# Kernel tuning notes

Measured on AMD Instinct MI355X. Metric: run time of the kernel, lower is better.

Reference implementation:

```python
import jax, jax.numpy as jnp
import numpy as np

B, S, D, H = 4, 2048, 1024, 16
DH = D // H


def setup_inputs() -> dict:
    key = jax.random.key(0)
    ks = jax.random.split(key, 11)
    s = 1.0 / np.sqrt(D)
    return {
        "q": jax.random.normal(ks[0], (B, S, D), jnp.float32),
        "k": jax.random.normal(ks[1], (B, S, D), jnp.float32),
        "v": jax.random.normal(ks[2], (B, S, D), jnp.float32),
        "Wq": jax.random.normal(ks[3], (D, D), jnp.float32) * s,
        "bq": jnp.zeros((D,), jnp.float32),
        "Wk": jax.random.normal(ks[4], (D, D), jnp.float32) * s,
        "bk": jnp.zeros((D,), jnp.float32),
        "Wv": jax.random.normal(ks[5], (D, D), jnp.float32) * s,
        "bv": jnp.zeros((D,), jnp.float32),
        "Wo": jax.random.normal(ks[6], (D, D), jnp.float32) * s,
        "bo": jnp.zeros((D,), jnp.float32),
    }


def _split_heads(x):
    # (B, S, D) -> (B, H, S, DH)
    b, s, _ = x.shape
    return x.reshape(b, s, H, DH).transpose(0, 2, 1, 3)


def reference(q, k, v, Wq, bq, Wk, bk, Wv, bv, Wo, bo):
    # torch Linear: x @ W.T + b
    qh = _split_heads(q @ Wq.T + bq)
    kh = _split_heads(k @ Wk.T + bk)
    vh = _split_heads(v @ Wv.T + bv)
    scale = 1.0 / jnp.sqrt(jnp.asarray(DH, qh.dtype))
    scores = jnp.einsum("bhqd,bhkd->bhqk", qh, kh) * scale  # (B,H,S,S)
    probs = jax.nn.softmax(scores, axis=-1)
    ctx = jnp.einsum("bhqk,bhkd->bhqd", probs, vh)  # (B,H,S,DH)
    x = ctx.transpose(0, 2, 1, 3).reshape(q.shape[0], -1, D)
    return x @ Wo.T + bo
```

## Files before the change

### kernel.cpp

```cpp
#include <hip/hip_runtime.h>

typedef __bf16 bf16x8 __attribute__((ext_vector_type(8)));
typedef __bf16 bf16x4 __attribute__((ext_vector_type(4)));
typedef _Float16 f16x8 __attribute__((ext_vector_type(8)));
typedef _Float16 f16x4v __attribute__((ext_vector_type(4)));
typedef float f32x4 __attribute__((ext_vector_type(4)));
typedef float f32x16 __attribute__((ext_vector_type(16)));
typedef unsigned short u16;
typedef unsigned int u32;
typedef unsigned int u32x4 __attribute__((ext_vector_type(4)));

constexpr int Bc = 4, Sc = 2048, Dc = 1024, Hc = 16, DHc = 64;
constexpr int Mrows = Bc * Sc;
constexpr size_t MK = (size_t)Mrows * Dc;
constexpr size_t WK = (size_t)Dc * Dc;

__device__ __forceinline__ u16 f2bf(float f) {
  u32 u = __float_as_uint(f);
  u = (u + 0x7fffu + ((u >> 16) & 1u)) >> 16;
  return (u16)u;
}

#define LDSP(p) ((__attribute__((address_space(3))) void*)(p))
#define GLBP(p) ((const __attribute__((address_space(1))) void*)(p))

__global__ __launch_bounds__(256) void cvt3_kernel(const float* __restrict__ a,
                                                   const float* __restrict__ b,
                                                   const float* __restrict__ c,
                                                   ushort4* __restrict__ out, int n4) {
  const float4* in = (const float4*)(blockIdx.y == 0 ? a : blockIdx.y == 1 ? b : c);
  ushort4* o = out + (size_t)blockIdx.y * n4;
  int stride = gridDim.x * blockDim.x;
  for (int i = blockIdx.x * blockDim.x + threadIdx.x; i < n4; i += stride) {
    float4 v = in[i];
    ushort4 r;
    r.x = f2bf(v.x); r.y = f2bf(v.y); r.z = f2bf(v.z); r.w = f2bf(v.w);
    o[i] = r;
  }
}

__global__ __launch_bounds__(256) void cvt4_kernel(const float* __restrict__ a,
                                                   const float* __restrict__ b,
                                                   const float* __restrict__ c,
                                                   const float* __restrict__ d,
                                                   ushort4* __restrict__ out, int n4) {
  const float4* in = (const float4*)(blockIdx.y == 0 ? a : blockIdx.y == 1 ? b
                                     : blockIdx.y == 2 ? c : d);
  ushort4* o = out + (size_t)blockIdx.y * n4;
  int stride = gridDim.x * blockDim.x;
  for (int i = blockIdx.x * blockDim.x + threadIdx.x; i < n4; i += stride) {
    float4 v = in[i];
    ushort4 r;
    r.x = f2bf(v.x); r.y = f2bf(v.y); r.z = f2bf(v.z); r.w = f2bf(v.w);
    o[i] = r;
  }
}

template <int FUSED3>
__global__ __launch_bounds__(512, 2) void gemm8(const u16* __restrict__ A0,
                                                const u16* __restrict__ Bt0,
                                                const float* __restrict__ b0,
                                                const float* __restrict__ b1,
                                                const float* __restrict__ b2,
                                                void* __restrict__ out0) {
  constexpr int K = 1024, NT = 16;
  __shared__ u16 lds[3 * 24576];

  const int y = FUSED3 ? (int)blockIdx.y : 3;
  const u16* A = A0 + (FUSED3 ? (size_t)blockIdx.y * MK : 0);
  const u16* Bt = Bt0 + (FUSED3 ? (size_t)blockIdx.y * WK : 0);
  const float* bias = FUSED3 ? (y == 0 ? b0 : y == 1 ? b1 : b2) : b0;

  const int wg = (blockIdx.x & 7) * 32 + (blockIdx.x >> 3);
  const int tm = wg >> 3, tn = wg & 7;
  const int row0 = tm << 8, col0 = tn << 7;

  const int t_ = threadIdx.x, w = t_ >> 6, l = t_ & 63;
  const int wm = w >> 1, wn = w & 1;
  const int col = l & 31, hh = l >> 5;

  f32x16 acc[2][2] = {};

  auto stA = [&](int tile, int i) {
    u16* buf = &lds[(tile % 3) * 24576];
    const int c = (w * 4 + i) * 64 + l;
    const int r = c >> 3, gl = c & 7;
    __builtin_amdgcn_global_load_lds(
        GLBP(A + (size_t)(row0 + r) * K + (tile << 6) + ((gl ^ (r & 7)) << 3)),
        LDSP(buf + (w * 4 + i) * 512), 16, 0, 0);
  };
  auto stB = [&](int tile, int i) {
    u16* buf = &lds[(tile % 3) * 24576] + 16384;
    const int c = (w * 2 + i) * 64 + l;
    const int r = c >> 3, gl = c & 7;
    __builtin_amdgcn_global_load_lds(
        GLBP(Bt + (size_t)(col0 + r) * K + (tile << 6) + ((gl ^ (r & 7)) << 3)),
        LDSP(buf + (w * 2 + i) * 512), 16, 0, 0);
  };

#pragma unroll
  for (int i = 0; i < 4; ++i) stA(0, i);
#pragma unroll
  for (int i = 0; i < 2; ++i) stB(0, i);
#pragma unroll
  for (int i = 0; i < 4; ++i) stA(1, i);
#pragma unroll
  for (int i = 0; i < 2; ++i) stB(1, i);
  asm volatile("s_waitcnt vmcnt(6)" ::: "memory");
  __builtin_amdgcn_s_barrier();

  const int ar0 = wm * 64 + col, ar1 = ar0 + 32;
  const int br0 = wn * 64 + col, br1 = br0 + 32;

#pragma unroll 1
  for (int t = 0; t < NT; ++t) {
    const u16* abuf = &lds[(t % 3) * 24576];
    const u16* bbuf = abuf + 16384;
#pragma unroll
    for (int ph = 0; ph < 2; ++ph) {
      bf16x8 a0[2], a1[2], q0[2], q1[2];
#pragma unroll
      for (int k2 = 0; k2 < 2; ++k2) {
        const int ks = ph * 2 + k2;
        a0[k2] = *(const bf16x8*)&abuf[ar0 * 64 + ((((ks << 1) + hh) ^ (ar0 & 7)) << 3)];
        a1[k2] = *(const bf16x8*)&abuf[ar1 * 64 + ((((ks << 1) + hh) ^ (ar1 & 7)) << 3)];
        q0[k2] = *(const bf16x8*)&bbuf[br0 * 64 + ((((ks << 1) + hh) ^ (br0 & 7)) << 3)];
        q1[k2] = *(const bf16x8*)&bbuf[br1 * 64 + ((((ks << 1) + hh) ^ (br1 & 7)) << 3)];
      }
      if (t + 2 < NT) {
        if (ph == 0) { stA(t + 2, 0); stA(t + 2, 1); stA(t + 2, 2); }
        else         { stA(t + 2, 3); stB(t + 2, 0); stB(t + 2, 1); }
      }
      __builtin_amdgcn_sched_barrier(0);
      __builtin_amdgcn_s_barrier();
      __builtin_amdgcn_sched_barrier(0);
      __builtin_amdgcn_s_setprio(1);
#pragma unroll
      for (int k2 = 0; k2 < 2; ++k2) {
        acc[0][0] = __builtin_amdgcn_mfma_f32_32x32x16_bf16(a0[k2], q0[k2], acc[0][0], 0, 0, 0);
        acc[0][1] = __builtin_amdgcn_mfma_f32_32x32x16_bf16(a0[k2], q1[k2], acc[0][1], 0, 0, 0);
        acc[1][0] = __builtin_amdgcn_mfma_f32_32x32x16_bf16(a1[k2], q0[k2], acc[1][0], 0, 0, 0);
        acc[1][1] = __builtin_amdgcn_mfma_f32_32x32x16_bf16(a1[k2], q1[k2], acc[1][1], 0, 0, 0);
      }
      __builtin_amdgcn_s_setprio(0);
      __builtin_amdgcn_sched_barrier(0);
    }
    if (t + 2 < NT)      asm volatile("s_waitcnt vmcnt(6)" ::: "memory");
    else if (t + 1 < NT) asm volatile("s_waitcnt vmcnt(0)" ::: "memory");
    __builtin_amdgcn_s_barrier();
  }

#pragma unroll
  for (int mi = 0; mi < 2; ++mi)
#pragma unroll
    for (int ni = 0; ni < 2; ++ni) {
      const int n = col0 + wn * 64 + ni * 32 + col;
      const float bv = bias[n];
      const int mbase = row0 + wm * 64 + mi * 32 + 4 * hh;
      if (y == 3) {
        float* O = (float*)out0;
#pragma unroll
        for (int r = 0; r < 16; ++r) {
          const int m = mbase + (r & 3) + 8 * (r >> 2);
          O[(size_t)m * Dc + n] = acc[mi][ni][r] + bv;
        }
      } else if (y == 2) {
        u16* Vt = (u16*)out0 + 2 * MK;
        const int h = n >> 6, dh = n & 63;
#pragma unroll
        for (int qg = 0; qg < 4; ++qg) {
          const int s0 = mbase + 8 * qg;
          const int b = s0 >> 11, s = s0 & (Sc - 1);
          f16x4v pk;
#pragma unroll
          for (int r4 = 0; r4 < 4; ++r4) pk[r4] = (_Float16)(acc[mi][ni][qg * 4 + r4] + bv);
          *(f16x4v*)&Vt[((size_t)((b * Hc + h) * DHc + dh)) * Sc + s] = pk;
        }
      } else {
        u16* Oh = (u16*)out0 + (size_t)y * MK;
        const float scl = (y == 0) ? 0.125f * 1.44269504089f : 1.f;
        const int h = n >> 6, dh = n & 63;
#pragma unroll
        for (int r = 0; r < 16; ++r) {
          const int m = mbase + (r & 3) + 8 * (r >> 2);
          const int b = m >> 11, s = m & (Sc - 1);
          Oh[((size_t)((b * Hc + h) * Sc + s)) * DHc + dh] = f2bf((acc[mi][ni][r] + bv) * scl);
        }
      }
    }
}

__global__ __launch_bounds__(256, 4) void attn4_kernel(const u16* __restrict__ Qh,
                                                       const u16* __restrict__ Kh,
                                                       const u16* __restrict__ Vt,
                                                       u16* __restrict__ ctx) {
  __shared__ u16 smem[16384];
  u16* K_lds = smem;
  u16* V_lds = smem + 8192;

  const int wid = (blockIdx.x & 7) * 128 + (blockIdx.x >> 3);
  const int qt = wid & 15, bh = wid >> 4;
  const int t = threadIdx.x, w = t >> 6, l = t & 63;
  const int q = l & 31, h = l >> 5;
  const int q0 = qt * 128 + w * 32;

  bf16x8 qf[4];
  {
    const u16* qp = Qh + ((size_t)bh * Sc + q0 + q) * DHc + h * 8;
#pragma unroll
    for (int kk = 0; kk < 4; ++kk) qf[kk] = *(const bf16x8*)(qp + kk * 16);
  }

  f32x16 oacc[2] = {};
  float m_run = -3.0e38f, l_run = 0.f;

  const int lrow = l >> 3, lg = l & 7;

  auto stage = [&](int tile, int buf) {
    const int kt = tile << 6;
    u16* Kb = K_lds + buf * 4096;
    u16* Vb = V_lds + buf * 4096;
#pragma unroll
    for (int c = 0; c < 2; ++c) {
      const int rb = w * 16 + c * 8;
      const int row = rb + lrow;
      const int sg = lg ^ (row & 7);
      __builtin_amdgcn_global_load_lds(GLBP(Kh + ((size_t)bh * Sc + kt + row) * DHc + sg * 8),
                                       LDSP(&Kb[rb * 64]), 16, 0, 0);
      __builtin_amdgcn_global_load_lds(GLBP(Vt + ((size_t)bh * DHc + row) * Sc + kt + sg * 8),
                                       LDSP(&Vb[rb * 64]), 16, 0, 0);
    }
  };

  stage(0, 0);
  __syncthreads();

#pragma unroll 1
  for (int tile = 0; tile < 32; ++tile) {
    const int cur = tile & 1;
    if (tile + 1 < 32) stage(tile + 1, cur ^ 1);
    const u16* Kb = K_lds + cur * 4096;
    const u16* Vb = V_lds + cur * 4096;

    f32x16 sacc[2] = {};
    __builtin_amdgcn_s_setprio(1);
#pragma unroll
    for (int kk = 0; kk < 4; ++kk) {
      const int kr0 = q, kr1 = 32 + q;
      bf16x8 kf0 = *(const bf16x8*)&Kb[kr0 * 64 + ((2 * kk + h) ^ (kr0 & 7)) * 8];
      bf16x8 kf1 = *(const bf16x8*)&Kb[kr1 * 64 + ((2 * kk + h) ^ (kr1 & 7)) * 8];
      sacc[0] = __builtin_amdgcn_mfma_f32_32x32x16_bf16(kf0, qf[kk], sacc[0], 0, 0, 0);
      sacc[1] = __builtin_amdgcn_mfma_f32_32x32x16_bf16(kf1, qf[kk], sacc[1], 0, 0, 0);
    }
    __builtin_amdgcn_s_setprio(0);

    float mx = sacc[0][0];
#pragma unroll
    for (int r = 1; r < 16; ++r) mx = fmaxf(mx, sacc[0][r]);
#pragma unroll
    for (int r = 0; r < 16; ++r) mx = fmaxf(mx, sacc[1][r]);
    mx = fmaxf(mx, __shfl_xor(mx, 32));
    if (__any(mx - m_run > 8.f)) {
      const float mnew = fmaxf(m_run, mx);
      const float corr = __builtin_amdgcn_exp2f(m_run - mnew);
      m_run = mnew;
      l_run *= corr;
#pragma unroll
      for (int dt = 0; dt < 2; ++dt)
#pragma unroll
        for (int r = 0; r < 16; ++r) oacc[dt][r] *= corr;
    }

    float sum = 0.f;
#pragma unroll
    for (int kt32 = 0; kt32 < 2; ++kt32)
#pragma unroll
      for (int c = 0; c < 2; ++c) {
        float p0 = __builtin_amdgcn_exp2f(sacc[kt32][c * 8 + 0] - m_run);
        float p1 = __builtin_amdgcn_exp2f(sacc[kt32][c * 8 + 1] - m_run);
        float p2 = __builtin_amdgcn_exp2f(sacc[kt32][c * 8 + 2] - m_run);
        float p3 = __builtin_amdgcn_exp2f(sacc[kt32][c * 8 + 3] - m_run);
        float p4 = __builtin_amdgcn_exp2f(sacc[kt32][c * 8 + 4] - m_run);
        float p5 = __builtin_amdgcn_exp2f(sacc[kt32][c * 8 + 5] - m_run);
        float p6 = __builtin_amdgcn_exp2f(sacc[kt32][c * 8 + 6] - m_run);
        float p7 = __builtin_amdgcn_exp2f(sacc[kt32][c * 8 + 7] - m_run);
        sum += ((p0 + p1) + (p2 + p3)) + ((p4 + p5) + (p6 + p7));
        u32 X0 = __builtin_bit_cast(u32, __builtin_amdgcn_cvt_pkrtz(p0, p1));
        u32 X1 = __builtin_bit_cast(u32, __builtin_amdgcn_cvt_pkrtz(p2, p3));
        u32 Y0 = __builtin_bit_cast(u32, __builtin_amdgcn_cvt_pkrtz(p4, p5));
        u32 Y1 = __builtin_bit_cast(u32, __builtin_amdgcn_cvt_pkrtz(p6, p7));
        auto rA = __builtin_amdgcn_permlane32_swap(X0, Y0, false, false);
        auto rB = __builtin_amdgcn_permlane32_swap(X1, Y1, false, false);
        u32x4 wv;
        wv[0] = rA[0]; wv[1] = rB[0]; wv[2] = rA[1]; wv[3] = rB[1];
        f16x8 pf = __builtin_bit_cast(f16x8, wv);
        const int gb = kt32 * 4 + c * 2 + h;
        __builtin_amdgcn_s_setprio(1);
#pragma unroll
        for (int dt = 0; dt < 2; ++dt) {
          const int vrow = dt * 32 + q;
          f16x8 vf = *(const f16x8*)&Vb[vrow * 64 + ((gb ^ (vrow & 7)) * 8)];
          oacc[dt] = __builtin_amdgcn_mfma_f32_32x32x16_f16(vf, pf, oacc[dt], 0, 0, 0);
        }
        __builtin_amdgcn_s_setprio(0);
      }
    sum += __shfl_xor(sum, 32);
    l_run += sum;
    __syncthreads();
  }

  const float inv = 1.f / l_run;
  u16* E = smem + w * 2048;
#pragma unroll
  for (int dt = 0; dt < 2; ++dt)
#pragma unroll
    for (int rg = 0; rg < 4; ++rg) {
      bf16x4 pk;
#pragma unroll
      for (int j = 0; j < 4; ++j) pk[j] = (__bf16)(oacc[dt][rg * 4 + j] * inv);
      const int dh0 = dt * 32 + rg * 8 + 4 * h;
      int byte = q * 128 + dh0 * 2;
      byte ^= (q & 7) << 4;
      *(bf16x4*)((char*)E + byte) = pk;
    }
  __syncthreads();
  const int b = bh >> 4, head = bh & 15;
  const size_t crow = ((size_t)(b * Sc + q0 + q)) * Dc + head * 64 + h * 32;
#pragma unroll
  for (int i = 0; i < 4; ++i) {
    const int g = (4 * h + i) ^ (q & 7);
    uint4 tv = *(const uint4*)((char*)E + q * 128 + g * 16);
    *(uint4*)((u16*)ctx + crow + i * 8) = tv;
  }
}

extern "C" void kernel_launch(void* const* d_in, const int* in_sizes, int n_in,
                              void* d_out, int out_size, void* d_ws, size_t ws_size,
                              hipStream_t stream) {
  const float* q  = (const float*)d_in[0];
  const float* k  = (const float*)d_in[1];
  const float* v  = (const float*)d_in[2];
  const float* Wq = (const float*)d_in[3];
  const float* bq = (const float*)d_in[4];
  const float* Wk = (const float*)d_in[5];
  const float* bk = (const float*)d_in[6];
  const float* Wv = (const float*)d_in[7];
  const float* bv = (const float*)d_in[8];
  const float* Wo = (const float*)d_in[9];
  const float* bo = (const float*)d_in[10];
  float* out = (float*)d_out;

  u16* qb  = (u16*)d_ws;
  u16* Wqb = qb + 3 * MK;
  u16* Qh  = Wqb + 4 * WK;
  u16* Kh  = Qh + MK;
  u16* VtB = Kh + MK;
  u16* ctx = VtB + MK;

  cvt3_kernel<<<dim3(2048, 3), 256, 0, stream>>>(q, k, v, (ushort4*)qb, (int)(MK / 4));
  cvt4_kernel<<<dim3(512, 4), 256, 0, stream>>>(Wq, Wk, Wv, Wo, (ushort4*)Wqb, (int)(WK / 4));

  gemm8<1><<<dim3(256, 3), 512, 0, stream>>>(qb, Wqb, bq, bk, bv, (void*)Qh);

  attn4_kernel<<<1024, 256, 0, stream>>>(Qh, Kh, VtB, ctx);

  gemm8<0><<<dim3(256, 1), 512, 0, stream>>>(ctx, Wqb + 3 * WK, bo, bo, bo, (void*)out);
}
```

Before: 220.5 us.

## Simplify GEMM mainloop to one barrier per tile; sum softmax probs via fdot2

The projection GEMM main loop drops its two-phase split with a mid-tile barrier. It now issues all prefetch loads for tile t+2 up front, reads all four k-slices of LDS fragments, then runs 16 MFMAs with one barrier per tile. This cuts barrier overhead but holds more fragment registers and may lose overlap of loads and compute. In attention, the row sum of exponentials uses fdot2 on the already-packed fp16 pairs instead of separate fp32 adds, which saves VALU work but sums rounded fp16 values.

```diff
diff --git a/kernel.cpp b/kernel.cpp
--- a/kernel.cpp
+++ b/kernel.cpp
@@ -4,6 +4,7 @@
 typedef __bf16 bf16x4 __attribute__((ext_vector_type(4)));
 typedef _Float16 f16x8 __attribute__((ext_vector_type(8)));
 typedef _Float16 f16x4v __attribute__((ext_vector_type(4)));
+typedef __fp16 fp16x2 __attribute__((ext_vector_type(2)));
 typedef float f32x4 __attribute__((ext_vector_type(4)));
 typedef float f32x16 __attribute__((ext_vector_type(16)));
 typedef unsigned short u16;
@@ -116,35 +117,27 @@
   for (int t = 0; t < NT; ++t) {
     const u16* abuf = &lds[(t % 3) * 24576];
     const u16* bbuf = abuf + 16384;
-#pragma unroll
-    for (int ph = 0; ph < 2; ++ph) {
-      bf16x8 a0[2], a1[2], q0[2], q1[2];
-#pragma unroll
-      for (int k2 = 0; k2 < 2; ++k2) {
-        const int ks = ph * 2 + k2;
-        a0[k2] = *(const bf16x8*)&abuf[ar0 * 64 + ((((ks << 1) + hh) ^ (ar0 & 7)) << 3)];
-        a1[k2] = *(const bf16x8*)&abuf[ar1 * 64 + ((((ks << 1) + hh) ^ (ar1 & 7)) << 3)];
-        q0[k2] = *(const bf16x8*)&bbuf[br0 * 64 + ((((ks << 1) + hh) ^ (br0 & 7)) << 3)];
-        q1[k2] = *(const bf16x8*)&bbuf[br1 * 64 + ((((ks << 1) + hh) ^ (br1 & 7)) << 3)];
-      }
-      if (t + 2 < NT) {
-        if (ph == 0) { stA(t + 2, 0); stA(t + 2, 1); stA(t + 2, 2); }
-        else         { stA(t + 2, 3); stB(t + 2, 0); stB(t + 2, 1); }
-      }
-      __builtin_amdgcn_sched_barrier(0);
-      __builtin_amdgcn_s_barrier();
-      __builtin_amdgcn_sched_barrier(0);
-      __builtin_amdgcn_s_setprio(1);
-#pragma unroll
-      for (int k2 = 0; k2 < 2; ++k2) {
-        acc[0][0] = __builtin_amdgcn_mfma_f32_32x32x16_bf16(a0[k2], q0[k2], acc[0][0], 0, 0, 0);
-        acc[0][1] = __builtin_amdgcn_mfma_f32_32x32x16_bf16(a0[k2], q1[k2], acc[0][1], 0, 0, 0);
-        acc[1][0] = __builtin_amdgcn_mfma_f32_32x32x16_bf16(a1[k2], q0[k2], acc[1][0], 0, 0, 0);
-        acc[1][1] = __builtin_amdgcn_mfma_f32_32x32x16_bf16(a1[k2], q1[k2], acc[1][1], 0, 0, 0);
-      }
-      __builtin_amdgcn_s_setprio(0);
-      __builtin_amdgcn_sched_barrier(0);
-    }
+    if (t + 2 < NT) {
+      stA(t + 2, 0); stA(t + 2, 1); stA(t + 2, 2); stA(t + 2, 3);
+      stB(t + 2, 0); stB(t + 2, 1);
+    }
+    bf16x8 af0[4], af1[4], bf0[4], bf1[4];
+#pragma unroll
+    for (int ks = 0; ks < 4; ++ks) {
+      af0[ks] = *(const bf16x8*)&abuf[ar0 * 64 + ((((ks << 1) + hh) ^ (ar0 & 7)) << 3)];
+      af1[ks] = *(const bf16x8*)&abuf[ar1 * 64 + ((((ks << 1) + hh) ^ (ar1 & 7)) << 3)];
+      bf0[ks] = *(const bf16x8*)&bbuf[br0 * 64 + ((((ks << 1) + hh) ^ (br0 & 7)) << 3)];
+      bf1[ks] = *(const bf16x8*)&bbuf[br1 * 64 + ((((ks << 1) + hh) ^ (br1 & 7)) << 3)];
+    }
+    __builtin_amdgcn_s_setprio(1);
+#pragma unroll
+    for (int ks = 0; ks < 4; ++ks) {
+      acc[0][0] = __builtin_amdgcn_mfma_f32_32x32x16_bf16(af0[ks], bf0[ks], acc[0][0], 0, 0, 0);
+      acc[0][1] = __builtin_amdgcn_mfma_f32_32x32x16_bf16(af0[ks], bf1[ks], acc[0][1], 0, 0, 0);
+      acc[1][0] = __builtin_amdgcn_mfma_f32_32x32x16_bf16(af1[ks], bf0[ks], acc[1][0], 0, 0, 0);
+      acc[1][1] = __builtin_amdgcn_mfma_f32_32x32x16_bf16(af1[ks], bf1[ks], acc[1][1], 0, 0, 0);
+    }
+    __builtin_amdgcn_s_setprio(0);
     if (t + 2 < NT)      asm volatile("s_waitcnt vmcnt(6)" ::: "memory");
     else if (t + 1 < NT) asm volatile("s_waitcnt vmcnt(0)" ::: "memory");
     __builtin_amdgcn_s_barrier();
@@ -213,6 +206,7 @@
 
   f32x16 oacc[2] = {};
   float m_run = -3.0e38f, l_run = 0.f;
+  const fp16x2 ones2 = {(__fp16)1.f, (__fp16)1.f};
 
   const int lrow = l >> 3, lg = l & 7;
 
@@ -271,7 +265,7 @@
         for (int r = 0; r < 16; ++r) oacc[dt][r] *= corr;
     }
 
-    float sum = 0.f;
+    float sumA = 0.f, sumB = 0.f;
 #pragma unroll
     for (int kt32 = 0; kt32 < 2; ++kt32)
 #pragma unroll
@@ -284,13 +278,18 @@
         float p5 = __builtin_amdgcn_exp2f(sacc[kt32][c * 8 + 5] - m_run);
         float p6 = __builtin_amdgcn_exp2f(sacc[kt32][c * 8 + 6] - m_run);
         float p7 = __builtin_amdgcn_exp2f(sacc[kt32][c * 8 + 7] - m_run);
-        sum += ((p0 + p1) + (p2 + p3)) + ((p4 + p5) + (p6 + p7));
-        u32 X0 = __builtin_bit_cast(u32, __builtin_amdgcn_cvt_pkrtz(p0, p1));
-        u32 X1 = __builtin_bit_cast(u32, __builtin_amdgcn_cvt_pkrtz(p2, p3));
-        u32 Y0 = __builtin_bit_cast(u32, __builtin_amdgcn_cvt_pkrtz(p4, p5));
-        u32 Y1 = __builtin_bit_cast(u32, __builtin_amdgcn_cvt_pkrtz(p6, p7));
-        auto rA = __builtin_amdgcn_permlane32_swap(X0, Y0, false, false);
-        auto rB = __builtin_amdgcn_permlane32_swap(X1, Y1, false, false);
+        fp16x2 X0 = __builtin_amdgcn_cvt_pkrtz(p0, p1);
+        fp16x2 X1 = __builtin_amdgcn_cvt_pkrtz(p2, p3);
+        fp16x2 Y0 = __builtin_amdgcn_cvt_pkrtz(p4, p5);
+        fp16x2 Y1 = __builtin_amdgcn_cvt_pkrtz(p6, p7);
+        sumA = __builtin_amdgcn_fdot2(X0, ones2, sumA, false);
+        sumA = __builtin_amdgcn_fdot2(X1, ones2, sumA, false);
+        sumB = __builtin_amdgcn_fdot2(Y0, ones2, sumB, false);
+        sumB = __builtin_amdgcn_fdot2(Y1, ones2, sumB, false);
+        auto rA = __builtin_amdgcn_permlane32_swap(__builtin_bit_cast(u32, X0),
+                                                   __builtin_bit_cast(u32, Y0), false, false);
+        auto rB = __builtin_amdgcn_permlane32_swap(__builtin_bit_cast(u32, X1),
+                                                   __builtin_bit_cast(u32, Y1), false, false);
         u32x4 wv;
         wv[0] = rA[0]; wv[1] = rB[0]; wv[2] = rA[1]; wv[3] = rB[1];
         f16x8 pf = __builtin_bit_cast(f16x8, wv);
@@ -304,6 +303,7 @@
         }
         __builtin_amdgcn_s_setprio(0);
       }
+    float sum = sumA + sumB;
     sum += __shfl_xor(sum, 32);
     l_run += sum;
     __syncthreads();
```

New measurement: 220.9 us. About the same (+0.2%).
